# Performance work log

Measured on AMD Instinct MI355X. Metric: run time of the kernel, lower is better.

## Reference

```python
import jax, jax.numpy as jnp
import numpy as np

B, T, D, U = 32, 2048, 128, 128


def setup_inputs() -> dict:
    key = jax.random.key(0)
    k1, k2, k3, k4 = jax.random.split(key, 4)
    x = jax.random.normal(k1, (B, T, D), dtype=jnp.float32)
    W_x = jax.random.normal(k2, (D, 4 * U), dtype=jnp.float32) * 0.05
    W_h = jax.random.normal(k3, (U, 4 * U), dtype=jnp.float32) * 0.05
    bias = jax.random.normal(k4, (4 * U,), dtype=jnp.float32) * 0.05
    return {"x": x, "W_x": W_x, "W_h": W_h, "bias": bias}


def reference(x, W_x, W_h, bias):
    # Keras gate order in the packed 4U dim: i, f, c(g), o
    u = W_h.shape[0]
    batch = x.shape[0]
    h0 = jnp.zeros((batch, u), dtype=x.dtype)
    c0 = jnp.zeros((batch, u), dtype=x.dtype)

    def step(carry, x_t):
        h, c = carry
        z = x_t @ W_x + h @ W_h + bias  # [B, 4U], fused 4-gate GEMM
        i = jax.nn.sigmoid(z[:, :u])
        f = jax.nn.sigmoid(z[:, u:2 * u])
        g = jnp.tanh(z[:, 2 * u:3 * u])
        o = jax.nn.sigmoid(z[:, 3 * u:])
        c_new = i * g + f * c
        h_new = o * jnp.tanh(c_new)
        return (h_new, c_new), h_new

    # scan over time: x -> [T, B, D]
    _, hs = jax.lax.scan(step, (h0, c0), jnp.swapaxes(x, 0, 1))
    return hs  # [T, B, U], matches original's np.array(h_sequences)
```

## Files before the change

### kernel.cpp

```cpp
#include <hip/hip_runtime.h>
#include <cstdint>
#include <cstddef>

#define B_ 32
#define T_ 2048
#define D_ 128
#define U_ 128
#define G4_ 512
#define P1_ROWS 32

typedef _Float16 h2v __attribute__((ext_vector_type(2)));

__device__ __forceinline__ float dot2f(h2v a, h2v b, float c) {
#if __has_builtin(__builtin_amdgcn_fdot2)
  return __builtin_amdgcn_fdot2(a, b, c, false);
#else
  return c + (float)a[0] * (float)b[0] + (float)a[1] * (float)b[1];
#endif
}

__global__ __launch_bounds__(512)
void zx_kernel(const float* __restrict__ x, const float* __restrict__ Wx,
               const float* __restrict__ bias, float* __restrict__ Zx,
               int tbase, int ct) {
  const int j = threadIdx.x;
  const int nt = ct / P1_ROWS;
  const int tblk = blockIdx.x % nt;
  const int b = blockIdx.x / nt;
  const int t0 = tblk * P1_ROWS;

  __shared__ float xsT[D_ * P1_ROWS];

  const float* xp = x + ((size_t)b * T_ + tbase + t0) * D_;
  {
    int e = j * 8;
    int r = e >> 7;
    int k = e & 127;
    float4 v0 = *(const float4*)(xp + e);
    float4 v1 = *(const float4*)(xp + e + 4);
    xsT[(k + 0) * P1_ROWS + r] = v0.x;
    xsT[(k + 1) * P1_ROWS + r] = v0.y;
    xsT[(k + 2) * P1_ROWS + r] = v0.z;
    xsT[(k + 3) * P1_ROWS + r] = v0.w;
    xsT[(k + 4) * P1_ROWS + r] = v1.x;
    xsT[(k + 5) * P1_ROWS + r] = v1.y;
    xsT[(k + 6) * P1_ROWS + r] = v1.z;
    xsT[(k + 7) * P1_ROWS + r] = v1.w;
  }
  __syncthreads();

  const float bj = bias[j];
  float acc[P1_ROWS];
#pragma unroll
  for (int r = 0; r < P1_ROWS; ++r) acc[r] = bj;

  const float* wp = Wx + j;
  float w = wp[0];
#pragma unroll 2
  for (int k = 0; k < D_; ++k) {
    float wn = (k + 1 < D_) ? wp[(size_t)(k + 1) * G4_] : 0.f;
    const float4* xr = (const float4*)(xsT + k * P1_ROWS);
#pragma unroll
    for (int r4 = 0; r4 < P1_ROWS / 4; ++r4) {
      float4 xv = xr[r4];
      acc[4 * r4 + 0] += xv.x * w;
      acc[4 * r4 + 1] += xv.y * w;
      acc[4 * r4 + 2] += xv.z * w;
      acc[4 * r4 + 3] += xv.w * w;
    }
    w = wn;
  }

  float* zp = Zx + ((size_t)t0 * B_ + b) * G4_ + j;
#pragma unroll
  for (int r = 0; r < P1_ROWS; ++r)
    zp[(size_t)r * B_ * G4_] = acc[r];
}

__global__ __launch_bounds__(512)
void lstm_kernel(const float* __restrict__ Zx, const float* __restrict__ Wh,
                 float* __restrict__ out, float* __restrict__ state,
                 int tbase, int ct, int first) {
  const int j = threadIdx.x;
  const int b = blockIdx.x;
  const int u = j & (U_ - 1);
  const int gate = j >> 7;

  h2v wh[64];
#pragma unroll
  for (int k2 = 0; k2 < 64; ++k2) {
    float w0 = Wh[(size_t)(2 * k2) * G4_ + j];
    float w1 = Wh[(size_t)(2 * k2 + 1) * G4_ + j];
    h2v p;
    p[0] = (_Float16)w0;
    p[1] = (_Float16)w1;
    wh[k2] = p;
  }

  __shared__ h2v hs[64];
  __shared__ float zs[G4_];

  float creg = 0.f;
  if (j < U_) {
    float h0 = 0.f;
    if (!first) {
      h0 = state[b * 2 * U_ + u];
      creg = state[b * 2 * U_ + U_ + u];
    }
    ((_Float16*)hs)[u] = (_Float16)h0;
  }
  __syncthreads();

  const float* zp = Zx + (size_t)b * G4_ + j;
  float zxc = zp[0];
  float hlast = 0.f;

  for (int t = 0; t < ct; ++t) {
    float zxn = (t + 1 < ct) ? zp[(size_t)(t + 1) * B_ * G4_] : 0.f;

    float a0 = 0.f, a1 = 0.f, a2 = 0.f, a3 = 0.f;
    const float4* hs4 = (const float4*)hs;
#pragma unroll
    for (int k8 = 0; k8 < 16; ++k8) {
      float4 hv = hs4[k8];
      a0 = dot2f(__builtin_bit_cast(h2v, hv.x), wh[4 * k8 + 0], a0);
      a1 = dot2f(__builtin_bit_cast(h2v, hv.y), wh[4 * k8 + 1], a1);
      a2 = dot2f(__builtin_bit_cast(h2v, hv.z), wh[4 * k8 + 2], a2);
      a3 = dot2f(__builtin_bit_cast(h2v, hv.w), wh[4 * k8 + 3], a3);
    }
    float z = zxc + ((a0 + a1) + (a2 + a3));

    float act;
    if (gate == 2) {
      act = 2.f / (1.f + __expf(-2.f * z)) - 1.f;
    } else {
      act = 1.f / (1.f + __expf(-z));
    }
    zs[j] = act;
    __syncthreads();

    if (j < U_) {
      float iv = zs[u];
      float fv = zs[u + 128];
      float gv = zs[u + 256];
      float ov = zs[u + 384];
      creg = iv * gv + fv * creg;
      float tc = 2.f / (1.f + __expf(-2.f * creg)) - 1.f;
      float hn = ov * tc;
      hlast = hn;
      out[((size_t)(tbase + t) * B_ + b) * U_ + u] = hn;
      ((_Float16*)hs)[u] = (_Float16)hn;
    }
    __syncthreads();
    zxc = zxn;
  }

  if (j < U_) {
    state[b * 2 * U_ + u] = hlast;
    state[b * 2 * U_ + U_ + u] = creg;
  }
}

extern "C" void kernel_launch(void* const* d_in, const int* in_sizes, int n_in,
                              void* d_out, int out_size, void* d_ws, size_t ws_size,
                              hipStream_t stream) {
  const float* x = (const float*)d_in[0];
  const float* Wx = (const float*)d_in[1];
  const float* Wh = (const float*)d_in[2];
  const float* bias = (const float*)d_in[3];
  float* out = (float*)d_out;

  float* state = (float*)d_ws;
  float* zx = (float*)((char*)d_ws + 32768);
  size_t avail = ws_size > 32768 ? ws_size - 32768 : 0;
  size_t per_t = (size_t)B_ * G4_ * sizeof(float);
  long maxct = (long)(avail / per_t);
  int ct;
  if (maxct >= T_) ct = T_;
  else {
    ct = (int)((maxct / P1_ROWS) * P1_ROWS);
    if (ct < P1_ROWS) ct = P1_ROWS;
  }

  for (int tb = 0; tb < T_; tb += ct) {
    int cur = (T_ - tb < ct) ? (T_ - tb) : ct;
    zx_kernel<<<dim3(B_ * (cur / P1_ROWS)), 512, 0, stream>>>(x, Wx, bias, zx, tb, cur);
    lstm_kernel<<<dim3(B_), 512, 0, stream>>>(zx, Wh, out, state, tb, cur, tb == 0 ? 1 : 0);
  }
}
```

Baseline: 1.424 ms.

## Split recurrent GEMV across quad lanes with DPP reduction and one barrier per step

Reorganizes the LSTM recurrence so each group of four lanes owns one hidden unit. Each lane computes partial dot products for all four gates over a quarter of K, then DPP quad permutes do a transpose-reduce and exchange the gate activations. This removes the shared-memory gate exchange, and a double-buffered h halves the per-step barriers to one. The Zx layout is also changed to time-contiguous per (batch, column), so the recurrent kernel can prefetch four timesteps with one float4 load. Every lane in the quad now computes the cell update redundantly, and the kernel relies on the assumption that ct is a multiple of 4.

```diff
diff --git a/kernel.cpp b/kernel.cpp
--- a/kernel.cpp
+++ b/kernel.cpp
@@ -18,6 +18,16 @@
   return c + (float)a[0] * (float)b[0] + (float)a[1] * (float)b[1];
 #endif
 }
+
+template <int CTRL>
+__device__ __forceinline__ float qperm(float x) {
+  return __builtin_bit_cast(
+      float, __builtin_amdgcn_mov_dpp(__builtin_bit_cast(int, x), CTRL, 0xF, 0xF, true));
+}
+#define XOR1_ 0xB1
+#define XOR2_ 0x4E
+#define XOR3_ 0x1B
+
 
 __global__ __launch_bounds__(512)
 void zx_kernel(const float* __restrict__ x, const float* __restrict__ Wx,
@@ -28,6 +38,7 @@
   const int tblk = blockIdx.x % nt;
   const int b = blockIdx.x / nt;
   const int t0 = tblk * P1_ROWS;
+  const int oc = (j & 3) * U_ + (j >> 2);
 
   __shared__ float xsT[D_ * P1_ROWS];
 
@@ -49,12 +60,12 @@
   }
   __syncthreads();
 
-  const float bj = bias[j];
+  const float bj = bias[oc];
   float acc[P1_ROWS];
 #pragma unroll
   for (int r = 0; r < P1_ROWS; ++r) acc[r] = bj;
 
-  const float* wp = Wx + j;
+  const float* wp = Wx + oc;
   float w = wp[0];
 #pragma unroll 2
   for (int k = 0; k < D_; ++k) {
@@ -71,10 +82,10 @@
     w = wn;
   }
 
-  float* zp = Zx + ((size_t)t0 * B_ + b) * G4_ + j;
-#pragma unroll
-  for (int r = 0; r < P1_ROWS; ++r)
-    zp[(size_t)r * B_ * G4_] = acc[r];
+  float* zp = Zx + ((size_t)b * G4_ + j) * ct + t0;
+#pragma unroll
+  for (int q = 0; q < P1_ROWS / 4; ++q)
+    ((float4*)zp)[q] = make_float4(acc[4 * q], acc[4 * q + 1], acc[4 * q + 2], acc[4 * q + 3]);
 }
 
 __global__ __launch_bounds__(512)
@@ -83,81 +94,104 @@
                  int tbase, int ct, int first) {
   const int j = threadIdx.x;
   const int b = blockIdx.x;
-  const int u = j & (U_ - 1);
-  const int gate = j >> 7;
-
-  h2v wh[64];
-#pragma unroll
-  for (int k2 = 0; k2 < 64; ++k2) {
-    float w0 = Wh[(size_t)(2 * k2) * G4_ + j];
-    float w1 = Wh[(size_t)(2 * k2 + 1) * G4_ + j];
+  const int u = j >> 2;
+  const int kq = j & 3;
+  const bool b0 = (kq & 1) != 0;
+  const bool b1 = (kq & 2) != 0;
+
+  h2v wh0[16], wh1[16], wh2[16], wh3[16];
+#pragma unroll
+  for (int k2 = 0; k2 < 16; ++k2) {
+    int k0 = kq * 32 + 2 * k2;
+    const float* w0p = Wh + (size_t)k0 * G4_;
+    const float* w1p = Wh + (size_t)(k0 + 1) * G4_;
     h2v p;
-    p[0] = (_Float16)w0;
-    p[1] = (_Float16)w1;
-    wh[k2] = p;
-  }
-
-  __shared__ h2v hs[64];
-  __shared__ float zs[G4_];
-
-  float creg = 0.f;
-  if (j < U_) {
-    float h0 = 0.f;
-    if (!first) {
-      h0 = state[b * 2 * U_ + u];
-      creg = state[b * 2 * U_ + U_ + u];
+    p[0] = (_Float16)w0p[0 * U_ + u]; p[1] = (_Float16)w1p[0 * U_ + u]; wh0[k2] = p;
+    p[0] = (_Float16)w0p[1 * U_ + u]; p[1] = (_Float16)w1p[1 * U_ + u]; wh1[k2] = p;
+    p[0] = (_Float16)w0p[2 * U_ + u]; p[1] = (_Float16)w1p[2 * U_ + u]; wh2[k2] = p;
+    p[0] = (_Float16)w0p[3 * U_ + u]; p[1] = (_Float16)w1p[3 * U_ + u]; wh3[k2] = p;
+  }
+
+  __shared__ h2v hbuf[2][64];
+
+  float c_state = 0.f, h0 = 0.f;
+  if (!first) {
+    h0 = state[b * 2 * U_ + u];
+    c_state = state[b * 2 * U_ + U_ + u];
+  }
+  if (kq == 0) ((_Float16*)hbuf[0])[u] = (_Float16)h0;
+  __syncthreads();
+
+  const float4* zx4 = (const float4*)(Zx + ((size_t)b * G4_ + j) * ct);
+  float4 zcur = zx4[0];
+  float hlast = h0;
+
+  for (int tt = 0; tt < ct; tt += 4) {
+    float4 znext = (tt + 4 < ct) ? zx4[(tt >> 2) + 1] : make_float4(0.f, 0.f, 0.f, 0.f);
+#pragma unroll
+    for (int s = 0; s < 4; ++s) {
+      const int t = tt + s;
+      const float zx_t = (s == 0) ? zcur.x : (s == 1) ? zcur.y : (s == 2) ? zcur.z : zcur.w;
+      const int cur = t & 1;
+
+      const float4* hp = (const float4*)((const char*)hbuf[cur] + kq * 64);
+      float p0 = 0.f, p1 = 0.f, p2 = 0.f, p3 = 0.f;
+#pragma unroll
+      for (int q4 = 0; q4 < 4; ++q4) {
+        float4 hv = hp[q4];
+        float hw[4] = {hv.x, hv.y, hv.z, hv.w};
+#pragma unroll
+        for (int e = 0; e < 4; ++e) {
+          h2v hh = __builtin_bit_cast(h2v, hw[e]);
+          int k2 = q4 * 4 + e;
+          p0 = dot2f(hh, wh0[k2], p0);
+          p1 = dot2f(hh, wh1[k2], p1);
+          p2 = dot2f(hh, wh2[k2], p2);
+          p3 = dot2f(hh, wh3[k2], p3);
+        }
+      }
+
+      float sx = b0 ? p0 : p1;
+      float sy = b0 ? p2 : p3;
+      float rx = qperm<XOR1_>(sx);
+      float ry = qperm<XOR1_>(sy);
+      float e0 = (b0 ? p1 : p0) + rx;
+      float e1 = (b0 ? p3 : p2) + ry;
+      float sz = b1 ? e0 : e1;
+      float rz = qperm<XOR2_>(sz);
+      float z = (b1 ? e1 : e0) + rz + zx_t;
+
+      const bool isg = (kq == 2);
+      float zz = isg ? z + z : z;
+      float ex = __expf(-zz);
+      float sg = __builtin_amdgcn_rcpf(1.f + ex);
+      float act = isg ? 2.f * sg - 1.f : sg;
+
+      float X1 = qperm<XOR1_>(act);
+      float X2 = qperm<XOR2_>(act);
+      float X3 = qperm<XOR3_>(act);
+      float ig = (b0 ? X1 : act) * (b0 ? X3 : X2);
+      float f_ = b0 ? (b1 ? X2 : act) : (b1 ? X3 : X1);
+      float o_ = b0 ? (b1 ? act : X2) : (b1 ? X1 : X3);
+
+      c_state = fmaf(f_, c_state, ig);
+      float e2 = __expf(-2.f * c_state);
+      float th = 2.f * __builtin_amdgcn_rcpf(1.f + e2) - 1.f;
+      float hn = o_ * th;
+      hlast = hn;
+
+      if (kq == 0) {
+        out[((size_t)(tbase + t) * B_ + b) * U_ + u] = hn;
+        ((_Float16*)hbuf[cur ^ 1])[u] = (_Float16)hn;
+      }
+      __syncthreads();
     }
-    ((_Float16*)hs)[u] = (_Float16)h0;
-  }
-  __syncthreads();
-
-  const float* zp = Zx + (size_t)b * G4_ + j;
-  float zxc = zp[0];
-  float hlast = 0.f;
-
-  for (int t = 0; t < ct; ++t) {
-    float zxn = (t + 1 < ct) ? zp[(size_t)(t + 1) * B_ * G4_] : 0.f;
-
-    float a0 = 0.f, a1 = 0.f, a2 = 0.f, a3 = 0.f;
-    const float4* hs4 = (const float4*)hs;
-#pragma unroll
-    for (int k8 = 0; k8 < 16; ++k8) {
-      float4 hv = hs4[k8];
-      a0 = dot2f(__builtin_bit_cast(h2v, hv.x), wh[4 * k8 + 0], a0);
-      a1 = dot2f(__builtin_bit_cast(h2v, hv.y), wh[4 * k8 + 1], a1);
-      a2 = dot2f(__builtin_bit_cast(h2v, hv.z), wh[4 * k8 + 2], a2);
-      a3 = dot2f(__builtin_bit_cast(h2v, hv.w), wh[4 * k8 + 3], a3);
-    }
-    float z = zxc + ((a0 + a1) + (a2 + a3));
-
-    float act;
-    if (gate == 2) {
-      act = 2.f / (1.f + __expf(-2.f * z)) - 1.f;
-    } else {
-      act = 1.f / (1.f + __expf(-z));
-    }
-    zs[j] = act;
-    __syncthreads();
-
-    if (j < U_) {
-      float iv = zs[u];
-      float fv = zs[u + 128];
-      float gv = zs[u + 256];
-      float ov = zs[u + 384];
-      creg = iv * gv + fv * creg;
-      float tc = 2.f / (1.f + __expf(-2.f * creg)) - 1.f;
-      float hn = ov * tc;
-      hlast = hn;
-      out[((size_t)(tbase + t) * B_ + b) * U_ + u] = hn;
-      ((_Float16*)hs)[u] = (_Float16)hn;
-    }
-    __syncthreads();
-    zxc = zxn;
-  }
-
-  if (j < U_) {
+    zcur = znext;
+  }
+
+  if (kq == 0) {
     state[b * 2 * U_ + u] = hlast;
-    state[b * 2 * U_ + U_ + u] = creg;
+    state[b * 2 * U_ + U_ + u] = c_state;
   }
 }
 
```

After: 1.240 ms. 1.15x faster.

## Use MFMA for recurrent matvec with per-wave gate ownership and double-buffered h

Applied to the files above, without the earlier changes.

Rewrites the recurrent step so each wave owns 16 hidden units across all four gates. It computes h@W_h with 16x16x32 f16 MFMA instructions, using a broadcast h as the A operand and W_h fragments held in registers. This removes the gate shuffle through shared memory and one of the two barriers per timestep, since h is double-buffered. The Zx layout is transposed to [b][gate][t] so each thread prefetches four timesteps with float4 loads, and sigmoid/tanh use a fast reciprocal. The cost is that MFMA work is wasted on the 15 redundant broadcast rows, and the transposed Zx writes are strided.

```diff
diff --git a/kernel.cpp b/kernel.cpp
--- a/kernel.cpp
+++ b/kernel.cpp
@@ -9,14 +9,14 @@
 #define G4_ 512
 #define P1_ROWS 32
 
-typedef _Float16 h2v __attribute__((ext_vector_type(2)));
-
-__device__ __forceinline__ float dot2f(h2v a, h2v b, float c) {
-#if __has_builtin(__builtin_amdgcn_fdot2)
-  return __builtin_amdgcn_fdot2(a, b, c, false);
-#else
-  return c + (float)a[0] * (float)b[0] + (float)a[1] * (float)b[1];
-#endif
+typedef _Float16 f16x8 __attribute__((ext_vector_type(8)));
+typedef float f32x4 __attribute__((ext_vector_type(4)));
+
+__device__ __forceinline__ float sigf(float z) {
+  return __builtin_amdgcn_rcpf(1.f + __expf(-z));
+}
+__device__ __forceinline__ float tanhf_(float z) {
+  return 2.f * __builtin_amdgcn_rcpf(1.f + __expf(-2.f * z)) - 1.f;
 }
 
 __global__ __launch_bounds__(512)
@@ -71,10 +71,10 @@
     w = wn;
   }
 
-  float* zp = Zx + ((size_t)t0 * B_ + b) * G4_ + j;
-#pragma unroll
-  for (int r = 0; r < P1_ROWS; ++r)
-    zp[(size_t)r * B_ * G4_] = acc[r];
+  float* zp = Zx + ((size_t)b * G4_ + j) * ct + t0;
+#pragma unroll
+  for (int q = 0; q < P1_ROWS / 4; ++q)
+    ((float4*)zp)[q] = make_float4(acc[4 * q], acc[4 * q + 1], acc[4 * q + 2], acc[4 * q + 3]);
 }
 
 __global__ __launch_bounds__(512)
@@ -83,81 +83,106 @@
                  int tbase, int ct, int first) {
   const int j = threadIdx.x;
   const int b = blockIdx.x;
-  const int u = j & (U_ - 1);
-  const int gate = j >> 7;
-
-  h2v wh[64];
-#pragma unroll
-  for (int k2 = 0; k2 < 64; ++k2) {
-    float w0 = Wh[(size_t)(2 * k2) * G4_ + j];
-    float w1 = Wh[(size_t)(2 * k2 + 1) * G4_ + j];
-    h2v p;
-    p[0] = (_Float16)w0;
-    p[1] = (_Float16)w1;
-    wh[k2] = p;
-  }
-
-  __shared__ h2v hs[64];
-  __shared__ float zs[G4_];
-
-  float creg = 0.f;
-  if (j < U_) {
-    float h0 = 0.f;
-    if (!first) {
-      h0 = state[b * 2 * U_ + u];
-      creg = state[b * 2 * U_ + U_ + u];
-    }
-    ((_Float16*)hs)[u] = (_Float16)h0;
-  }
+  const int w = j >> 6;
+  const int lane = j & 63;
+  const int l4 = lane & 15;
+  const int kg = lane >> 4;
+  const int u = w * 16 + l4;
+
+  f16x8 bf[4][4];
+#pragma unroll
+  for (int g = 0; g < 4; ++g)
+#pragma unroll
+    for (int kt = 0; kt < 4; ++kt) {
+      f16x8 v;
+#pragma unroll
+      for (int e = 0; e < 8; ++e)
+        v[e] = (_Float16)Wh[(size_t)(kt * 32 + kg * 8 + e) * G4_ + g * U_ + u];
+      bf[g][kt] = v;
+    }
+
+  __shared__ alignas(16) _Float16 hbuf[2][U_];
+
+  float c_state = 0.f, h0 = 0.f;
+  if (!first) {
+    h0 = state[b * 2 * U_ + u];
+    c_state = state[b * 2 * U_ + U_ + u];
+  }
+  if (kg == 0) hbuf[0][u] = (_Float16)h0;
   __syncthreads();
 
-  const float* zp = Zx + (size_t)b * G4_ + j;
-  float zxc = zp[0];
-  float hlast = 0.f;
-
-  for (int t = 0; t < ct; ++t) {
-    float zxn = (t + 1 < ct) ? zp[(size_t)(t + 1) * B_ * G4_] : 0.f;
-
-    float a0 = 0.f, a1 = 0.f, a2 = 0.f, a3 = 0.f;
-    const float4* hs4 = (const float4*)hs;
-#pragma unroll
-    for (int k8 = 0; k8 < 16; ++k8) {
-      float4 hv = hs4[k8];
-      a0 = dot2f(__builtin_bit_cast(h2v, hv.x), wh[4 * k8 + 0], a0);
-      a1 = dot2f(__builtin_bit_cast(h2v, hv.y), wh[4 * k8 + 1], a1);
-      a2 = dot2f(__builtin_bit_cast(h2v, hv.z), wh[4 * k8 + 2], a2);
-      a3 = dot2f(__builtin_bit_cast(h2v, hv.w), wh[4 * k8 + 3], a3);
-    }
-    float z = zxc + ((a0 + a1) + (a2 + a3));
-
-    float act;
-    if (gate == 2) {
-      act = 2.f / (1.f + __expf(-2.f * z)) - 1.f;
+  const float4* zq0 = (const float4*)(Zx + ((size_t)b * G4_ + 0 * U_ + u) * ct);
+  const float4* zq1 = (const float4*)(Zx + ((size_t)b * G4_ + 1 * U_ + u) * ct);
+  const float4* zq2 = (const float4*)(Zx + ((size_t)b * G4_ + 2 * U_ + u) * ct);
+  const float4* zq3 = (const float4*)(Zx + ((size_t)b * G4_ + 3 * U_ + u) * ct);
+
+  float4 zc0 = zq0[0], zc1 = zq1[0], zc2 = zq2[0], zc3 = zq3[0];
+  float hlast = h0;
+
+  for (int tt = 0; tt < ct; tt += 4) {
+    float4 zn0, zn1, zn2, zn3;
+    if (tt + 4 < ct) {
+      const int nq = (tt >> 2) + 1;
+      zn0 = zq0[nq]; zn1 = zq1[nq]; zn2 = zq2[nq]; zn3 = zq3[nq];
     } else {
-      act = 1.f / (1.f + __expf(-z));
-    }
-    zs[j] = act;
-    __syncthreads();
-
-    if (j < U_) {
-      float iv = zs[u];
-      float fv = zs[u + 128];
-      float gv = zs[u + 256];
-      float ov = zs[u + 384];
-      creg = iv * gv + fv * creg;
-      float tc = 2.f / (1.f + __expf(-2.f * creg)) - 1.f;
-      float hn = ov * tc;
+      zn0 = zn1 = zn2 = zn3 = make_float4(0.f, 0.f, 0.f, 0.f);
+    }
+#pragma unroll
+    for (int s = 0; s < 4; ++s) {
+      const int t = tt + s;
+      const int cur = t & 1;
+      const float zi0 = (s == 0) ? zc0.x : (s == 1) ? zc0.y : (s == 2) ? zc0.z : zc0.w;
+      const float zi1 = (s == 0) ? zc1.x : (s == 1) ? zc1.y : (s == 2) ? zc1.z : zc1.w;
+      const float zi2 = (s == 0) ? zc2.x : (s == 1) ? zc2.y : (s == 2) ? zc2.z : zc2.w;
+      const float zi3 = (s == 0) ? zc3.x : (s == 1) ? zc3.y : (s == 2) ? zc3.z : zc3.w;
+
+      const f16x8* hp = (const f16x8*)hbuf[cur];
+      f16x8 a0 = hp[0 * 4 + kg];
+      f16x8 a1 = hp[1 * 4 + kg];
+      f16x8 a2 = hp[2 * 4 + kg];
+      f16x8 a3 = hp[3 * 4 + kg];
+
+      f32x4 acc0 = {zi0, zi0, zi0, zi0};
+      f32x4 acc1 = {zi1, zi1, zi1, zi1};
+      f32x4 acc2 = {zi2, zi2, zi2, zi2};
+      f32x4 acc3 = {zi3, zi3, zi3, zi3};
+      acc0 = __builtin_amdgcn_mfma_f32_16x16x32_f16(a0, bf[0][0], acc0, 0, 0, 0);
+      acc1 = __builtin_amdgcn_mfma_f32_16x16x32_f16(a0, bf[1][0], acc1, 0, 0, 0);
+      acc2 = __builtin_amdgcn_mfma_f32_16x16x32_f16(a0, bf[2][0], acc2, 0, 0, 0);
+      acc3 = __builtin_amdgcn_mfma_f32_16x16x32_f16(a0, bf[3][0], acc3, 0, 0, 0);
+      acc0 = __builtin_amdgcn_mfma_f32_16x16x32_f16(a1, bf[0][1], acc0, 0, 0, 0);
+      acc1 = __builtin_amdgcn_mfma_f32_16x16x32_f16(a1, bf[1][1], acc1, 0, 0, 0);
+      acc2 = __builtin_amdgcn_mfma_f32_16x16x32_f16(a1, bf[2][1], acc2, 0, 0, 0);
+      acc3 = __builtin_amdgcn_mfma_f32_16x16x32_f16(a1, bf[3][1], acc3, 0, 0, 0);
+      acc0 = __builtin_amdgcn_mfma_f32_16x16x32_f16(a2, bf[0][2], acc0, 0, 0, 0);
+      acc1 = __builtin_amdgcn_mfma_f32_16x16x32_f16(a2, bf[1][2], acc1, 0, 0, 0);
+      acc2 = __builtin_amdgcn_mfma_f32_16x16x32_f16(a2, bf[2][2], acc2, 0, 0, 0);
+      acc3 = __builtin_amdgcn_mfma_f32_16x16x32_f16(a2, bf[3][2], acc3, 0, 0, 0);
+      acc0 = __builtin_amdgcn_mfma_f32_16x16x32_f16(a3, bf[0][3], acc0, 0, 0, 0);
+      acc1 = __builtin_amdgcn_mfma_f32_16x16x32_f16(a3, bf[1][3], acc1, 0, 0, 0);
+      acc2 = __builtin_amdgcn_mfma_f32_16x16x32_f16(a3, bf[2][3], acc2, 0, 0, 0);
+      acc3 = __builtin_amdgcn_mfma_f32_16x16x32_f16(a3, bf[3][3], acc3, 0, 0, 0);
+
+      float i_ = sigf(acc0[0]);
+      float f_ = sigf(acc1[0]);
+      float g_ = tanhf_(acc2[0]);
+      float o_ = sigf(acc3[0]);
+      c_state = fmaf(f_, c_state, i_ * g_);
+      float hn = o_ * tanhf_(c_state);
       hlast = hn;
-      out[((size_t)(tbase + t) * B_ + b) * U_ + u] = hn;
-      ((_Float16*)hs)[u] = (_Float16)hn;
-    }
-    __syncthreads();
-    zxc = zxn;
-  }
-
-  if (j < U_) {
+
+      if (kg == 0) {
+        out[((size_t)(tbase + t) * B_ + b) * U_ + u] = hn;
+        hbuf[cur ^ 1][u] = (_Float16)hn;
+      }
+      __syncthreads();
+    }
+    zc0 = zn0; zc1 = zn1; zc2 = zn2; zc3 = zn3;
+  }
+
+  if (kg == 0) {
     state[b * 2 * U_ + u] = hlast;
-    state[b * 2 * U_ + U_ + u] = creg;
+    state[b * 2 * U_ + U_ + u] = c_state;
   }
 }
 
```

Result: faster. 1.196 ms (-16.0%).
